# Kernel optimization log

Measured on AMD Instinct MI355X. Metric: run time of the kernel, lower is better.

Reference implementation:

```python
import jax, jax.numpy as jnp
import numpy as np

# Transformer-XL relative multi-head attention (eval mode, dropout = identity)
B, Q, M, D, H = 2, 1024, 1024, 1024, 16
DH = D // H          # 64 head dim
K = Q + M            # key length = memory + current segment
SCALE = 0.02         # param init scale


def setup_inputs() -> dict:
    key = jax.random.key(0)
    ks = jax.random.split(key, 10)
    return {
        "inputs": jax.random.normal(ks[0], (B, Q, D), jnp.float32),
        "inputs_mem": jax.random.normal(ks[1], (B, M, D), jnp.float32),
        "r": jax.random.normal(ks[2], (B, K, D), jnp.float32),
        "W_qkv": jax.random.normal(ks[3], (D, 3 * D), jnp.float32) * SCALE,
        "b_qkv": jnp.zeros((3 * D,), jnp.float32),
        "W_r": jax.random.normal(ks[4], (D, D), jnp.float32) * SCALE,
        "b_r": jnp.zeros((D,), jnp.float32),
        "W_o": jax.random.normal(ks[5], (D, D), jnp.float32) * SCALE,
        "b_o": jnp.zeros((D,), jnp.float32),
        "u": jax.random.normal(ks[6], (1, H, 1, DH), jnp.float32) * SCALE,
        "v": jax.random.normal(ks[7], (1, H, 1, DH), jnp.float32) * SCALE,
    }


def _split_heads(x):
    # [B, L, D] -> [B, H, L, DH]
    b, l, _ = x.shape
    return x.reshape(b, l, H, DH).transpose(0, 2, 1, 3)


def _rel_shift(x):
    # Transformer-XL relative shift: pad one zero column on the left,
    # reshape to [B, H, K+1, Q], drop first row, reshape back.
    b, h, q, k = x.shape
    x = jnp.pad(x, ((0, 0), (0, 0), (0, 0), (1, 0)))
    x = x.reshape(b, h, k + 1, q)[:, :, 1:, :]
    return x.reshape(b, h, q, k)


def reference(inputs, inputs_mem, r, W_qkv, b_qkv, W_r, b_r, W_o, b_o, u, v):
    cat = jnp.concatenate([inputs_mem, inputs], axis=1)      # [B, K, D]
    w = cat @ W_qkv + b_qkv                                   # [B, K, 3D]
    rp = r @ W_r + b_r                                        # [B, K, D]
    # NOTE: source splits as (q, v, k) in that order
    w_q, w_v, w_k = jnp.split(w, 3, axis=-1)
    hq = _split_heads(w_q)[:, :, -Q:]                          # [B, H, Q, DH]
    hk = _split_heads(w_k)                                     # [B, H, K, DH]
    hv = _split_heads(w_v)                                     # [B, H, K, DH]
    hr = _split_heads(rp)                                      # [B, H, K, DH]
    ac = jnp.einsum('bhqd,bhkd->bhqk', hq + u, hk)             # content term
    bd = _rel_shift(jnp.einsum('bhqd,bhkd->bhqk', hq + v, hr)) # position term
    score = (ac + bd) / (DH ** 0.5)
    # causal mask with memory: query i attends to all mem + positions <= i
    mem_len = K - Q
    mask = (jnp.arange(K)[None, :] <= mem_len + jnp.arange(Q)[:, None]).astype(jnp.float32)
    score = score * mask - 1e30 * (1.0 - mask)
    weights = jax.nn.softmax(score, axis=-1)                   # [B, H, Q, K]
    out = jnp.einsum('bhqk,bhkd->bhqd', weights, hv)           # [B, H, Q, DH]
    out = out.transpose(0, 2, 1, 3).reshape(B, Q, D)
    return out @ W_o + b_o
```

## Files before the change

kernel.cpp:

```cpp
#include <hip/hip_runtime.h>
#include <hip/hip_bf16.h>
#include <stdint.h>


typedef __bf16 bf16;
typedef __bf16 bf16x2 __attribute__((ext_vector_type(2)));
typedef __bf16 bf16x4 __attribute__((ext_vector_type(4)));
typedef __bf16 bf16x8 __attribute__((ext_vector_type(8)));
typedef float  f32x4  __attribute__((ext_vector_type(4)));

__device__ __forceinline__ void async_copy16(void* lds, const void* g) {
    auto gp = (const __attribute__((address_space(1))) void*)(uintptr_t)g;
    auto lp = (__attribute__((address_space(3))) void*)(uint32_t)(uintptr_t)lds;
    __builtin_amdgcn_global_load_lds(gp, lp, 16, 0, 0);
}

__device__ __forceinline__ void gemm128_core(
    const bf16* __restrict__ A, const bf16* __restrict__ Bt, const int Kd,
    const int m0, const int n0, bf16* As, bf16* Bs, f32x4 acc[4][4])
{
    const int tid  = threadIdx.x;
    const int lane = tid & 63;
    const int wave = tid >> 6;
    const int wr   = (wave >> 1) * 64;
    const int wc   = (wave & 1) * 64;
    const int lr   = lane & 15;
    const int q4   = lane >> 4;

#pragma unroll
    for (int i = 0; i < 4; ++i)
#pragma unroll
        for (int j = 0; j < 4; ++j) {
            acc[i][j][0] = 0.f; acc[i][j][1] = 0.f; acc[i][j][2] = 0.f; acc[i][j][3] = 0.f;
        }

    for (int k0 = 0; k0 < Kd; k0 += 32) {
#pragma unroll
        for (int it = 0; it < 2; ++it) {
            const int cb0   = (it * 4 + wave) * 64;
            const int chunk = cb0 + lane;
            const int row   = chunk >> 2;
            const int cg    = (chunk & 3) * 8;
            async_copy16(As + cb0 * 8, A  + (size_t)(m0 + row) * Kd + k0 + cg);
            async_copy16(Bs + cb0 * 8, Bt + (size_t)(n0 + row) * Kd + k0 + cg);
        }
        __syncthreads();
        bf16x8 af[4], bfr[4];
#pragma unroll
        for (int rb = 0; rb < 4; ++rb)
            af[rb] = *(const bf16x8*)&As[(wr + rb * 16 + lr) * 32 + q4 * 8];
#pragma unroll
        for (int cb = 0; cb < 4; ++cb)
            bfr[cb] = *(const bf16x8*)&Bs[(wc + cb * 16 + lr) * 32 + q4 * 8];
#pragma unroll
        for (int rb = 0; rb < 4; ++rb)
#pragma unroll
            for (int cb = 0; cb < 4; ++cb)
                acc[rb][cb] = __builtin_amdgcn_mfma_f32_16x16x32_bf16(af[rb], bfr[cb], acc[rb][cb], 0, 0, 0);
        __syncthreads();
    }
}

__device__ __forceinline__ void gemm64_core(
    const bf16* __restrict__ A, const bf16* __restrict__ Bt, const int Kd,
    const int m0, const int n0, bf16* As, bf16* Bs, f32x4 acc[2][4])
{
    const int tid  = threadIdx.x;
    const int lane = tid & 63;
    const int wave = tid >> 6;
    const int wr   = (wave >> 1) * 32;
    const int wc   = (wave & 1) * 64;
    const int lr   = lane & 15;
    const int q4   = lane >> 4;

#pragma unroll
    for (int i = 0; i < 2; ++i)
#pragma unroll
        for (int j = 0; j < 4; ++j) {
            acc[i][j][0] = 0.f; acc[i][j][1] = 0.f; acc[i][j][2] = 0.f; acc[i][j][3] = 0.f;
        }

    for (int k0 = 0; k0 < Kd; k0 += 32) {
        {
            const int chunk = tid;
            const int row   = chunk >> 2;
            const int cg    = (chunk & 3) * 8;
            async_copy16(As + (wave * 64) * 8, A + (size_t)(m0 + row) * Kd + k0 + cg);
        }
#pragma unroll
        for (int it = 0; it < 2; ++it) {
            const int cb0   = (it * 4 + wave) * 64;
            const int chunk = cb0 + lane;
            const int row   = chunk >> 2;
            const int cg    = (chunk & 3) * 8;
            async_copy16(Bs + cb0 * 8, Bt + (size_t)(n0 + row) * Kd + k0 + cg);
        }
        __syncthreads();
        bf16x8 af[2], bfr[4];
#pragma unroll
        for (int rb = 0; rb < 2; ++rb)
            af[rb] = *(const bf16x8*)&As[(wr + rb * 16 + lr) * 32 + q4 * 8];
#pragma unroll
        for (int cb = 0; cb < 4; ++cb)
            bfr[cb] = *(const bf16x8*)&Bs[(wc + cb * 16 + lr) * 32 + q4 * 8];
#pragma unroll
        for (int rb = 0; rb < 2; ++rb)
#pragma unroll
            for (int cb = 0; cb < 4; ++cb)
                acc[rb][cb] = __builtin_amdgcn_mfma_f32_16x16x32_bf16(af[rb], bfr[cb], acc[rb][cb], 0, 0, 0);
        __syncthreads();
    }
}

__global__ __launch_bounds__(256) void k_prep_w(
    const float* __restrict__ Wqkv, const float* __restrict__ Wr,
    const float* __restrict__ Wo,
    bf16* __restrict__ Wqkvt, bf16* __restrict__ Wrt, bf16* __restrict__ Wot)
{
    __shared__ float t[32][33];
    int id = blockIdx.x;
    const float* in; bf16* out; int C, bx, by;
    if (id < 3072)      { in = Wqkv; out = Wqkvt; C = 3072; bx = id % 96; by = id / 96; }
    else if (id < 4096) { id -= 3072; in = Wr; out = Wrt; C = 1024; bx = id & 31; by = id >> 5; }
    else                { id -= 4096; in = Wo; out = Wot; C = 1024; bx = id & 31; by = id >> 5; }
    const int R = 1024;
    const int c0 = bx * 32, r0 = by * 32;
    const int lc = threadIdx.x & 31, lrow = threadIdx.x >> 5;
#pragma unroll
    for (int p = 0; p < 4; ++p)
        t[lrow + p * 8][lc] = in[(size_t)(r0 + lrow + p * 8) * C + c0 + lc];
    __syncthreads();
#pragma unroll
    for (int p = 0; p < 4; ++p)
        out[(size_t)(c0 + lrow + p * 8) * R + r0 + lc] = (bf16)t[lc][lrow + p * 8];
}

__global__ __launch_bounds__(256) void k_prep_x(
    const float* __restrict__ mem, const float* __restrict__ inp,
    const float* __restrict__ r,
    bf16* __restrict__ catb, bf16* __restrict__ rb)
{
    const int id = blockIdx.x;
    if (id < 4096) {
        const int e   = (id * 256 + threadIdx.x) * 4;
        const int row = e >> 10, dc = e & 1023;
        const int b   = row >> 11, k = row & 2047;
        const float* src = (k < 1024) ? mem + ((size_t)b * 1024 + k) * 1024 + dc
                                      : inp + ((size_t)b * 1024 + (k - 1024)) * 1024 + dc;
        float4 f = *(const float4*)src;
        bf16x4 o; o[0] = (bf16)f.x; o[1] = (bf16)f.y; o[2] = (bf16)f.z; o[3] = (bf16)f.w;
        *(bf16x4*)&catb[e] = o;
    } else {
        const int e = ((id - 4096) * 256 + threadIdx.x) * 4;
        float4 f = *(const float4*)(r + e);
        bf16x4 o; o[0] = (bf16)f.x; o[1] = (bf16)f.y; o[2] = (bf16)f.z; o[3] = (bf16)f.w;
        *(bf16x4*)&rb[e] = o;
    }
}

__global__ __launch_bounds__(256) void k_gemm_qkvr(
    const bf16* __restrict__ catb, const bf16* __restrict__ Wqkvt,
    const float* __restrict__ b_qkv, const float* __restrict__ u, const float* __restrict__ v,
    const bf16* __restrict__ rb_, const bf16* __restrict__ Wrt,
    const float* __restrict__ b_r,
    bf16* __restrict__ hq_u, bf16* __restrict__ hq_v,
    bf16* __restrict__ hk, bf16* __restrict__ hvT, bf16* __restrict__ hr)
{
    __shared__ bf16 lds[2 * 128 * 32];
    f32x4 acc[4][4];
    const int lane = threadIdx.x & 63, wave = threadIdx.x >> 6;
    const int wr = (wave >> 1) * 64, wc = (wave & 1) * 64;
    const int lr = lane & 15, q4 = lane >> 4;
    const int y = blockIdx.y;

    if (y < 16) {
        const int m0 = blockIdx.x * 128;
        const int n0 = 1024 + y * 128;
        gemm128_core(catb, Wqkvt, 1024, m0, n0, lds, lds + 128 * 32, acc);
#pragma unroll
        for (int rb = 0; rb < 4; ++rb) {
#pragma unroll
            for (int cb = 0; cb < 4; ++cb) {
                const int col  = n0 + wc + cb * 16 + lr;
                const int part = col >> 10;
                const int hd   = col & 1023;
                const int h    = hd >> 6, d = hd & 63;
                const float bcol = b_qkv[col];
#pragma unroll
                for (int r = 0; r < 4; ++r) {
                    const int row = m0 + wr + rb * 16 + q4 * 4 + r;
                    const int b   = row >> 11, k = row & 2047;
                    const float val = acc[rb][cb][r] + bcol;
                    if (part == 1) {
                        hvT[(((size_t)(b * 16 + h)) * 64 + d) * 2048 + k] = (bf16)val;
                    } else {
                        hk[(((size_t)(b * 16 + h)) * 2048 + k) * 64 + d] = (bf16)val;
                    }
                }
            }
        }
    } else if (y < 20) {
        const int linear = (y - 16) * 32 + blockIdx.x;
        const int n0 = (linear & 7) * 128;
        const int mi = linear >> 3;
        const int m0 = (mi >> 3) * 2048 + 1024 + (mi & 7) * 128;
        gemm128_core(catb, Wqkvt, 1024, m0, n0, lds, lds + 128 * 32, acc);
#pragma unroll
        for (int rb = 0; rb < 4; ++rb) {
#pragma unroll
            for (int cb = 0; cb < 4; ++cb) {
                const int col = n0 + wc + cb * 16 + lr;
                const int h = col >> 6, d = col & 63;
                const float bcol = b_qkv[col];
                const float uc = u[col], vc = v[col];
#pragma unroll
                for (int r = 0; r < 4; ++r) {
                    const int row = m0 + wr + rb * 16 + q4 * 4 + r;
                    const int b   = row >> 11, k = row & 2047;
                    const float val = acc[rb][cb][r] + bcol;
                    const size_t o = (((size_t)(b * 16 + h)) * 1024 + (k - 1024)) * 64 + d;
                    hq_u[o] = (bf16)(val + uc);
                    hq_v[o] = (bf16)(val + vc);
                }
            }
        }
    } else {
        const int m0 = blockIdx.x * 128;
        const int n0 = (y - 20) * 128;
        gemm128_core(rb_, Wrt, 1024, m0, n0, lds, lds + 128 * 32, acc);
#pragma unroll
        for (int rb = 0; rb < 4; ++rb) {
#pragma unroll
            for (int cb = 0; cb < 4; ++cb) {
                const int col = n0 + wc + cb * 16 + lr;
                const int h = col >> 6, d = col & 63;
                const float bcol = b_r[col];
#pragma unroll
                for (int r = 0; r < 4; ++r) {
                    const int row = m0 + wr + rb * 16 + q4 * 4 + r;
                    const int b = row >> 11, k = row & 2047;
                    hr[(((size_t)(b * 16 + h)) * 2048 + k) * 64 + d] = (bf16)(acc[rb][cb][r] + bcol);
                }
            }
        }
    }
}

__global__ __launch_bounds__(256) void k_gemm_out(
    const bf16* __restrict__ attn, const bf16* __restrict__ Wt,
    const float* __restrict__ bias, float* __restrict__ out)
{
    __shared__ bf16 lds[64 * 32 + 128 * 32];
    f32x4 acc[2][4];
    const int m0 = blockIdx.x * 64, n0 = blockIdx.y * 128;
    gemm64_core(attn, Wt, 1024, m0, n0, lds, lds + 64 * 32, acc);

    const int lane = threadIdx.x & 63, wave = threadIdx.x >> 6;
    const int wr = (wave >> 1) * 32, wc = (wave & 1) * 64;
    const int lr = lane & 15, q4 = lane >> 4;
#pragma unroll
    for (int rb = 0; rb < 2; ++rb) {
#pragma unroll
        for (int cb = 0; cb < 4; ++cb) {
            const int col = n0 + wc + cb * 16 + lr;
            const float bcol = bias[col];
#pragma unroll
            for (int r = 0; r < 4; ++r) {
                const int row = m0 + wr + rb * 16 + q4 * 4 + r;
                out[(size_t)row * 1024 + col] = acc[rb][cb][r] + bcol;
            }
        }
    }
}

__global__ __launch_bounds__(256) void k_attn(
    const bf16* __restrict__ hq_u, const bf16* __restrict__ hq_v,
    const bf16* __restrict__ hk, const bf16* __restrict__ hvT,
    const bf16* __restrict__ hr, bf16* __restrict__ attn)
{
    __shared__ bf16 Ks[2][64][72];
    __shared__ bf16 Vt[2][64][72];
    __shared__ bf16 Rs[192 * 72];
    __shared__ bf16 U[4][1600];

    const int bh = blockIdx.y;
    const int qt = (bh & 16) ? (15 - (int)blockIdx.x) : (int)blockIdx.x;
    const int q0 = qt * 64;
    const int tid = threadIdx.x, lane = tid & 63, wave = tid >> 6;
    const int lr = lane & 15, q4 = lane >> 4;
    bf16* Uw = &U[wave][0];

    const int nt  = 17 + qt;
    const int m0c = 15 - qt;
    const size_t kvbase = (size_t)bh * 2048 * 64;

    const int ci0  = tid,        r0_ = ci0 >> 3,  c0_ = (ci0 & 7) * 8;
    const int ci1  = 256 + tid,  r1_ = ci1 >> 3,  c1_ = (ci1 & 7) * 8;

    bf16x8 kv0, kv1, vv0, vv1, rv0, rv1;
    auto load_kv = [&](int t) {
        const int k0 = t * 64;
        kv0 = *(const bf16x8*)&hk [kvbase + (size_t)(k0 + r0_) * 64 + c0_];
        kv1 = *(const bf16x8*)&hk [kvbase + (size_t)(k0 + r1_) * 64 + c1_];
        vv0 = *(const bf16x8*)&hvT[kvbase + (size_t)r0_ * 2048 + k0 + c0_];
        vv1 = *(const bf16x8*)&hvT[kvbase + (size_t)r1_ * 2048 + k0 + c1_];
    };
    auto load_r = [&](int c) {
        if (c * 64 < 2048) {
            rv0 = *(const bf16x8*)&hr[kvbase + (size_t)(c * 64 + r0_) * 64 + c0_];
            rv1 = *(const bf16x8*)&hr[kvbase + (size_t)(c * 64 + r1_) * 64 + c1_];
        } else {
#pragma unroll
            for (int z = 0; z < 8; ++z) { rv0[z] = (bf16)0.f; rv1[z] = (bf16)0.f; }
        }
    };
    auto write_kv = [&](int buf) {
        *(bf16x8*)&Ks[buf][r0_][c0_] = kv0;
        *(bf16x8*)&Ks[buf][r1_][c1_] = kv1;
        *(bf16x8*)&Vt[buf][r0_][c0_] = vv0;
        *(bf16x8*)&Vt[buf][r1_][c1_] = vv1;
    };
    auto write_r = [&](int slot) {
        *(bf16x8*)&Rs[(slot * 64 + r0_) * 72 + c0_] = rv0;
        *(bf16x8*)&Rs[(slot * 64 + r1_) * 72 + c1_] = rv1;
    };

    const size_t qrow = ((size_t)bh * 1024 + q0 + wave * 16 + lr) * 64;
    const bf16x8 qu0 = *(const bf16x8*)&hq_u[qrow + q4 * 8];
    const bf16x8 qu1 = *(const bf16x8*)&hq_u[qrow + 32 + q4 * 8];
    const bf16x8 qv0 = *(const bf16x8*)&hq_v[qrow + q4 * 8];
    const bf16x8 qv1 = *(const bf16x8*)&hq_v[qrow + 32 + q4 * 8];

    f32x4 Oacc[4];
#pragma unroll
    for (int i = 0; i < 4; ++i) { Oacc[i][0] = 0.f; Oacc[i][1] = 0.f; Oacc[i][2] = 0.f; Oacc[i][3] = 0.f; }
    float lp[4] = {0.f, 0.f, 0.f, 0.f};

    load_kv(0);  write_kv(0);
    load_r(m0c);     write_r(m0c % 3);
    load_r(m0c + 1); write_r((m0c + 1) % 3);
    __syncthreads();

    for (int t = 0; t < nt; ++t) {
        const int k0  = t * 64;
        const int mt  = m0c + t;
        const int s0  = mt % 3;
        const int s1  = (s0 + 1 == 3) ? 0 : s0 + 1;
        const int s2  = (s1 + 1 == 3) ? 0 : s1 + 1;
        const int buf = t & 1;
        const bool more = (t + 1 < nt);
        if (more) { load_kv(t + 1); load_r(mt + 2); }

        __builtin_amdgcn_s_setprio(1);
        f32x4 S[4];
#pragma unroll
        for (int cb = 0; cb < 4; ++cb) {
            const bf16x8 kf0 = *(const bf16x8*)&Ks[buf][cb * 16 + lr][q4 * 8];
            const bf16x8 kf1 = *(const bf16x8*)&Ks[buf][cb * 16 + lr][32 + q4 * 8];
            f32x4 z; z[0] = 0.f; z[1] = 0.f; z[2] = 0.f; z[3] = 0.f;
            z = __builtin_amdgcn_mfma_f32_16x16x32_bf16(qu0, kf0, z, 0, 0, 0);
            S[cb] = __builtin_amdgcn_mfma_f32_16x16x32_bf16(qu1, kf1, z, 0, 0, 0);
        }
#pragma unroll
        for (int jbi = 0; jbi < 5; ++jbi) {
            const int jb   = jbi + 3 - wave;
            const int rrow = ((jb & 4) ? s1 : s0) * 64 + (jb & 3) * 16 + lr;
            const bf16x8 rf0 = *(const bf16x8*)&Rs[rrow * 72 + q4 * 8];
            const bf16x8 rf1 = *(const bf16x8*)&Rs[rrow * 72 + 32 + q4 * 8];
            f32x4 z; z[0] = 0.f; z[1] = 0.f; z[2] = 0.f; z[3] = 0.f;
            z = __builtin_amdgcn_mfma_f32_16x16x32_bf16(qv0, rf0, z, 0, 0, 0);
            z = __builtin_amdgcn_mfma_f32_16x16x32_bf16(qv1, rf1, z, 0, 0, 0);
            bf16x4 pk;
            pk[0] = (bf16)z[0]; pk[1] = (bf16)z[1]; pk[2] = (bf16)z[2]; pk[3] = (bf16)z[3];
            *(bf16x4*)&Uw[(jbi * 16 + lr) * 20 + q4 * 4] = pk;
        }

        float bdv[4][4];
#pragma unroll
        for (int cb = 0; cb < 4; ++cb)
#pragma unroll
            for (int r = 0; r < 4; ++r) {
                const int tq = q4 * 4 + r;
                bdv[cb][r] = (float)Uw[(cb * 16 + lr + 15 - tq) * 20 + tq];
            }

#pragma unroll
        for (int cb = 0; cb < 4; ++cb) {
            const int k = k0 + cb * 16 + lr;
#pragma unroll
            for (int r = 0; r < 4; ++r) {
                const int q = q0 + wave * 16 + q4 * 4 + r;
                const float s = (S[cb][r] + bdv[cb][r]) * 0.125f;
                const float p = (k <= 1024 + q) ? __expf(s) : 0.f;
                lp[r] += p;
                Uw[(q4 * 4 + r) * 76 + cb * 16 + lr] = (bf16)p;
            }
        }

        const bf16x8 pf0 = *(const bf16x8*)&Uw[lr * 76 + q4 * 8];
        const bf16x8 pf1 = *(const bf16x8*)&Uw[lr * 76 + 32 + q4 * 8];
#pragma unroll
        for (int db = 0; db < 4; ++db) {
            const bf16x8 vf0 = *(const bf16x8*)&Vt[buf][db * 16 + lr][q4 * 8];
            const bf16x8 vf1 = *(const bf16x8*)&Vt[buf][db * 16 + lr][32 + q4 * 8];
            Oacc[db] = __builtin_amdgcn_mfma_f32_16x16x32_bf16(pf0, vf0, Oacc[db], 0, 0, 0);
            Oacc[db] = __builtin_amdgcn_mfma_f32_16x16x32_bf16(pf1, vf1, Oacc[db], 0, 0, 0);
        }
        __builtin_amdgcn_s_setprio(0);

        if (more) {
            write_kv(buf ^ 1);
            write_r(s2);
            __syncthreads();
        }
    }

#pragma unroll
    for (int off = 1; off < 16; off <<= 1)
#pragma unroll
        for (int r = 0; r < 4; ++r) lp[r] += __shfl_xor(lp[r], off, 64);

    const int b = bh >> 4, h = bh & 15;
#pragma unroll
    for (int r = 0; r < 4; ++r) {
        const float rl = 1.f / lp[r];
        const int q = q0 + wave * 16 + q4 * 4 + r;
#pragma unroll
        for (int db = 0; db < 4; ++db) {
            const int d = db * 16 + lr;
            attn[(((size_t)b * 1024 + q) * 16 + h) * 64 + d] = (bf16)(Oacc[db][r] * rl);
        }
    }
}

extern "C" void kernel_launch(void* const* d_in, const int* in_sizes, int n_in,
                              void* d_out, int out_size, void* d_ws, size_t ws_size,
                              hipStream_t stream)
{
    const float* inputs = (const float*)d_in[0];
    const float* mem    = (const float*)d_in[1];
    const float* r      = (const float*)d_in[2];
    const float* W_qkv  = (const float*)d_in[3];
    const float* b_qkv  = (const float*)d_in[4];
    const float* W_r    = (const float*)d_in[5];
    const float* b_r    = (const float*)d_in[6];
    const float* W_o    = (const float*)d_in[7];
    const float* b_o    = (const float*)d_in[8];
    const float* u      = (const float*)d_in[9];
    const float* v      = (const float*)d_in[10];
    float* out = (float*)d_out;

    char* ws = (char*)d_ws;
    size_t off = 0;
    auto alloc = [&](size_t bytes) -> void* {
        void* p = ws + off;
        off += (bytes + 255) & ~(size_t)255;
        return p;
    };
    bf16* hq_u  = (bf16*)alloc(2ull * 16 * 1024 * 64 * 2);
    bf16* hq_v  = (bf16*)alloc(2ull * 16 * 1024 * 64 * 2);
    bf16* hk    = (bf16*)alloc(2ull * 16 * 2048 * 64 * 2);
    bf16* hvT   = (bf16*)alloc(2ull * 16 * 2048 * 64 * 2);
    bf16* hr    = (bf16*)alloc(2ull * 16 * 2048 * 64 * 2);
    bf16* attnb = (bf16*)alloc(2ull * 1024 * 1024 * 2);
    bf16* Wot   = (bf16*)alloc(1024ull * 1024 * 2);
    bf16* catb  = (bf16*)alloc(4096ull * 1024 * 2);
    bf16* rb    = (bf16*)alloc(4096ull * 1024 * 2);
    bf16* Wqkvt = (bf16*)alloc(3072ull * 1024 * 2);
    bf16* Wrt   = (bf16*)alloc(1024ull * 1024 * 2);

    k_prep_w<<<5120, 256, 0, stream>>>(W_qkv, W_r, W_o, Wqkvt, Wrt, Wot);
    k_prep_x<<<8192, 256, 0, stream>>>(mem, inputs, r, catb, rb);

    k_gemm_qkvr<<<dim3(32, 28), 256, 0, stream>>>(catb, Wqkvt, b_qkv, u, v,
                                                  rb, Wrt, b_r,
                                                  hq_u, hq_v, hk, hvT, hr);
    k_attn<<<dim3(16, 32), 256, 0, stream>>>(hq_u, hq_v, hk, hvT, hr, attnb);
    k_gemm_out<<<dim3(32, 8), 256, 0, stream>>>(attnb, Wot, b_o, out);
}
```

Baseline: 249.9 us.

## Double-buffer LDS tiles in GEMM cores and merge prep kernels

Both GEMM cores now ping-pong between two LDS buffers: the global-to-LDS async copy for the next K-slice is issued before the MFMA work on the current slice, so load latency can overlap compute. This drops one barrier per iteration and doubles the LDS footprint per block, which may lower occupancy. The separate weight-transpose and activation-cast prep kernels are also merged into a single launch to cut launch overhead.

```diff
diff --git a/kernel.cpp b/kernel.cpp
--- a/kernel.cpp
+++ b/kernel.cpp
@@ -34,24 +34,35 @@
             acc[i][j][0] = 0.f; acc[i][j][1] = 0.f; acc[i][j][2] = 0.f; acc[i][j][3] = 0.f;
         }
 
-    for (int k0 = 0; k0 < Kd; k0 += 32) {
+    auto stage = [&](int buf, int k0) {
 #pragma unroll
         for (int it = 0; it < 2; ++it) {
             const int cb0   = (it * 4 + wave) * 64;
             const int chunk = cb0 + lane;
             const int row   = chunk >> 2;
             const int cg    = (chunk & 3) * 8;
-            async_copy16(As + cb0 * 8, A  + (size_t)(m0 + row) * Kd + k0 + cg);
-            async_copy16(Bs + cb0 * 8, Bt + (size_t)(n0 + row) * Kd + k0 + cg);
-        }
-        __syncthreads();
+            async_copy16(As + buf * 4096 + cb0 * 8, A  + (size_t)(m0 + row) * Kd + k0 + cg);
+            async_copy16(Bs + buf * 4096 + cb0 * 8, Bt + (size_t)(n0 + row) * Kd + k0 + cg);
+        }
+    };
+
+    const int NT = Kd >> 5;
+    stage(0, 0);
+    __syncthreads();
+
+    for (int t = 0; t < NT; ++t) {
+        const int buf = t & 1;
+        if (t + 1 < NT) stage(buf ^ 1, (t + 1) * 32);
+
+        const bf16* Ab = As + buf * 4096;
+        const bf16* Bb = Bs + buf * 4096;
         bf16x8 af[4], bfr[4];
 #pragma unroll
         for (int rb = 0; rb < 4; ++rb)
-            af[rb] = *(const bf16x8*)&As[(wr + rb * 16 + lr) * 32 + q4 * 8];
+            af[rb] = *(const bf16x8*)&Ab[(wr + rb * 16 + lr) * 32 + q4 * 8];
 #pragma unroll
         for (int cb = 0; cb < 4; ++cb)
-            bfr[cb] = *(const bf16x8*)&Bs[(wc + cb * 16 + lr) * 32 + q4 * 8];
+            bfr[cb] = *(const bf16x8*)&Bb[(wc + cb * 16 + lr) * 32 + q4 * 8];
 #pragma unroll
         for (int rb = 0; rb < 4; ++rb)
 #pragma unroll
@@ -80,12 +91,12 @@
             acc[i][j][0] = 0.f; acc[i][j][1] = 0.f; acc[i][j][2] = 0.f; acc[i][j][3] = 0.f;
         }
 
-    for (int k0 = 0; k0 < Kd; k0 += 32) {
+    auto stage = [&](int buf, int k0) {
         {
             const int chunk = tid;
             const int row   = chunk >> 2;
             const int cg    = (chunk & 3) * 8;
-            async_copy16(As + (wave * 64) * 8, A + (size_t)(m0 + row) * Kd + k0 + cg);
+            async_copy16(As + buf * 2048 + (wave * 64) * 8, A + (size_t)(m0 + row) * Kd + k0 + cg);
         }
 #pragma unroll
         for (int it = 0; it < 2; ++it) {
@@ -93,16 +104,27 @@
             const int chunk = cb0 + lane;
             const int row   = chunk >> 2;
             const int cg    = (chunk & 3) * 8;
-            async_copy16(Bs + cb0 * 8, Bt + (size_t)(n0 + row) * Kd + k0 + cg);
-        }
-        __syncthreads();
+            async_copy16(Bs + buf * 4096 + cb0 * 8, Bt + (size_t)(n0 + row) * Kd + k0 + cg);
+        }
+    };
+
+    const int NT = Kd >> 5;
+    stage(0, 0);
+    __syncthreads();
+
+    for (int t = 0; t < NT; ++t) {
+        const int buf = t & 1;
+        if (t + 1 < NT) stage(buf ^ 1, (t + 1) * 32);
+
+        const bf16* Ab = As + buf * 2048;
+        const bf16* Bb = Bs + buf * 4096;
         bf16x8 af[2], bfr[4];
 #pragma unroll
         for (int rb = 0; rb < 2; ++rb)
-            af[rb] = *(const bf16x8*)&As[(wr + rb * 16 + lr) * 32 + q4 * 8];
+            af[rb] = *(const bf16x8*)&Ab[(wr + rb * 16 + lr) * 32 + q4 * 8];
 #pragma unroll
         for (int cb = 0; cb < 4; ++cb)
-            bfr[cb] = *(const bf16x8*)&Bs[(wc + cb * 16 + lr) * 32 + q4 * 8];
+            bfr[cb] = *(const bf16x8*)&Bb[(wc + cb * 16 + lr) * 32 + q4 * 8];
 #pragma unroll
         for (int rb = 0; rb < 2; ++rb)
 #pragma unroll
@@ -112,37 +134,33 @@
     }
 }
 
-__global__ __launch_bounds__(256) void k_prep_w(
+__global__ __launch_bounds__(256) void k_prep(
     const float* __restrict__ Wqkv, const float* __restrict__ Wr,
     const float* __restrict__ Wo,
-    bf16* __restrict__ Wqkvt, bf16* __restrict__ Wrt, bf16* __restrict__ Wot)
+    const float* __restrict__ mem, const float* __restrict__ inp,
+    const float* __restrict__ r,
+    bf16* __restrict__ Wqkvt, bf16* __restrict__ Wrt, bf16* __restrict__ Wot,
+    bf16* __restrict__ catb, bf16* __restrict__ rb)
 {
     __shared__ float t[32][33];
     int id = blockIdx.x;
-    const float* in; bf16* out; int C, bx, by;
-    if (id < 3072)      { in = Wqkv; out = Wqkvt; C = 3072; bx = id % 96; by = id / 96; }
-    else if (id < 4096) { id -= 3072; in = Wr; out = Wrt; C = 1024; bx = id & 31; by = id >> 5; }
-    else                { id -= 4096; in = Wo; out = Wot; C = 1024; bx = id & 31; by = id >> 5; }
-    const int R = 1024;
-    const int c0 = bx * 32, r0 = by * 32;
-    const int lc = threadIdx.x & 31, lrow = threadIdx.x >> 5;
-#pragma unroll
-    for (int p = 0; p < 4; ++p)
-        t[lrow + p * 8][lc] = in[(size_t)(r0 + lrow + p * 8) * C + c0 + lc];
-    __syncthreads();
-#pragma unroll
-    for (int p = 0; p < 4; ++p)
-        out[(size_t)(c0 + lrow + p * 8) * R + r0 + lc] = (bf16)t[lc][lrow + p * 8];
-}
-
-__global__ __launch_bounds__(256) void k_prep_x(
-    const float* __restrict__ mem, const float* __restrict__ inp,
-    const float* __restrict__ r,
-    bf16* __restrict__ catb, bf16* __restrict__ rb)
-{
-    const int id = blockIdx.x;
-    if (id < 4096) {
-        const int e   = (id * 256 + threadIdx.x) * 4;
+    if (id < 5120) {
+        const float* in; bf16* out; int C, bx, by;
+        if (id < 3072)      { in = Wqkv; out = Wqkvt; C = 3072; bx = id % 96; by = id / 96; }
+        else if (id < 4096) { id -= 3072; in = Wr; out = Wrt; C = 1024; bx = id & 31; by = id >> 5; }
+        else                { id -= 4096; in = Wo; out = Wot; C = 1024; bx = id & 31; by = id >> 5; }
+        const int R = 1024;
+        const int c0 = bx * 32, r0 = by * 32;
+        const int lc = threadIdx.x & 31, lrow = threadIdx.x >> 5;
+#pragma unroll
+        for (int p = 0; p < 4; ++p)
+            t[lrow + p * 8][lc] = in[(size_t)(r0 + lrow + p * 8) * C + c0 + lc];
+        __syncthreads();
+#pragma unroll
+        for (int p = 0; p < 4; ++p)
+            out[(size_t)(c0 + lrow + p * 8) * R + r0 + lc] = (bf16)t[lc][lrow + p * 8];
+    } else if (id < 9216) {
+        const int e   = ((id - 5120) * 256 + threadIdx.x) * 4;
         const int row = e >> 10, dc = e & 1023;
         const int b   = row >> 11, k = row & 2047;
         const float* src = (k < 1024) ? mem + ((size_t)b * 1024 + k) * 1024 + dc
@@ -151,7 +169,7 @@
         bf16x4 o; o[0] = (bf16)f.x; o[1] = (bf16)f.y; o[2] = (bf16)f.z; o[3] = (bf16)f.w;
         *(bf16x4*)&catb[e] = o;
     } else {
-        const int e = ((id - 4096) * 256 + threadIdx.x) * 4;
+        const int e = ((id - 9216) * 256 + threadIdx.x) * 4;
         float4 f = *(const float4*)(r + e);
         bf16x4 o; o[0] = (bf16)f.x; o[1] = (bf16)f.y; o[2] = (bf16)f.z; o[3] = (bf16)f.w;
         *(bf16x4*)&rb[e] = o;
@@ -166,7 +184,7 @@
     bf16* __restrict__ hq_u, bf16* __restrict__ hq_v,
     bf16* __restrict__ hk, bf16* __restrict__ hvT, bf16* __restrict__ hr)
 {
-    __shared__ bf16 lds[2 * 128 * 32];
+    __shared__ bf16 lds[4 * 128 * 32];
     f32x4 acc[4][4];
     const int lane = threadIdx.x & 63, wave = threadIdx.x >> 6;
     const int wr = (wave >> 1) * 64, wc = (wave & 1) * 64;
@@ -176,7 +194,7 @@
     if (y < 16) {
         const int m0 = blockIdx.x * 128;
         const int n0 = 1024 + y * 128;
-        gemm128_core(catb, Wqkvt, 1024, m0, n0, lds, lds + 128 * 32, acc);
+        gemm128_core(catb, Wqkvt, 1024, m0, n0, lds, lds + 2 * 4096, acc);
 #pragma unroll
         for (int rb = 0; rb < 4; ++rb) {
 #pragma unroll
@@ -204,7 +222,7 @@
         const int n0 = (linear & 7) * 128;
         const int mi = linear >> 3;
         const int m0 = (mi >> 3) * 2048 + 1024 + (mi & 7) * 128;
-        gemm128_core(catb, Wqkvt, 1024, m0, n0, lds, lds + 128 * 32, acc);
+        gemm128_core(catb, Wqkvt, 1024, m0, n0, lds, lds + 2 * 4096, acc);
 #pragma unroll
         for (int rb = 0; rb < 4; ++rb) {
 #pragma unroll
@@ -227,7 +245,7 @@
     } else {
         const int m0 = blockIdx.x * 128;
         const int n0 = (y - 20) * 128;
-        gemm128_core(rb_, Wrt, 1024, m0, n0, lds, lds + 128 * 32, acc);
+        gemm128_core(rb_, Wrt, 1024, m0, n0, lds, lds + 2 * 4096, acc);
 #pragma unroll
         for (int rb = 0; rb < 4; ++rb) {
 #pragma unroll
@@ -250,10 +268,10 @@
     const bf16* __restrict__ attn, const bf16* __restrict__ Wt,
     const float* __restrict__ bias, float* __restrict__ out)
 {
-    __shared__ bf16 lds[64 * 32 + 128 * 32];
+    __shared__ bf16 lds[2 * 2048 + 2 * 4096];
     f32x4 acc[2][4];
     const int m0 = blockIdx.x * 64, n0 = blockIdx.y * 128;
-    gemm64_core(attn, Wt, 1024, m0, n0, lds, lds + 64 * 32, acc);
+    gemm64_core(attn, Wt, 1024, m0, n0, lds, lds + 2 * 2048, acc);
 
     const int lane = threadIdx.x & 63, wave = threadIdx.x >> 6;
     const int wr = (wave >> 1) * 32, wc = (wave & 1) * 64;
@@ -469,8 +487,8 @@
     bf16* Wqkvt = (bf16*)alloc(3072ull * 1024 * 2);
     bf16* Wrt   = (bf16*)alloc(1024ull * 1024 * 2);
 
-    k_prep_w<<<5120, 256, 0, stream>>>(W_qkv, W_r, W_o, Wqkvt, Wrt, Wot);
-    k_prep_x<<<8192, 256, 0, stream>>>(mem, inputs, r, catb, rb);
+    k_prep<<<13312, 256, 0, stream>>>(W_qkv, W_r, W_o, mem, inputs, r,
+                                      Wqkvt, Wrt, Wot, catb, rb);
 
     k_gemm_qkvr<<<dim3(32, 28), 256, 0, stream>>>(catb, Wqkvt, b_qkv, u, v,
                                                   rb, Wrt, b_r,
```

Result: no change. 248.8 us (-0.4%).
